# Performance work log

Measured on AMD Instinct MI355X. Metric: run time of the kernel, lower is better.

The kernel has to match this reference:

```python
import jax, jax.numpy as jnp
import numpy as np

B, D = 8192, 512
NB_CLASSES = 11318
N_EXP = 16
POS_THRESH = 0.25
TOP_K = int(round(B * POS_THRESH))  # plan==1: k = round(B * pos_thresh)


def make_bweights(n):
    # Deterministic init_bweights() from the torch module (17x17 for n=16).
    bw = np.zeros((n + 1, n + 1), dtype=np.float32)
    bw[:, 0] = -1.0 / n
    bw[0, 0] = 1.0
    for i in range(1, n + 1):
        for j in range(1, i):
            bw[i, j] = (-1.0 / n - bw[i] @ bw[j]) / bw[j, j]
        bw[i, i] = np.sqrt(1.0 - np.sum(bw[i, : i + 1] ** 2))
    bw[-1, -1] = 0.0
    return bw


def setup_inputs() -> dict:
    key = jax.random.key(0)
    k1, k2, k3, k4 = jax.random.split(key, 4)
    x_batch = jax.random.normal(k1, (B, D), jnp.float32)
    y_batch = jax.random.randint(k2, (B,), 0, NB_CLASSES)
    # kaiming_normal_ mode='fan_out' on a [nb_classes, sz_embed] tensor: std=sqrt(2/nb_classes)
    proxies = jax.random.normal(k3, (NB_CLASSES, D), jnp.float32) * np.float32(np.sqrt(2.0 / NB_CLASSES))
    rand_units = jax.random.normal(k4, (TOP_K, N_EXP, D), jnp.float32)
    rand_units = rand_units / jnp.linalg.norm(rand_units, axis=-1, keepdims=True)  # gen_unit()
    bweights = jnp.asarray(make_bweights(N_EXP))
    return {"x_batch": x_batch, "y_batch": y_batch, "proxies": proxies,
            "bweights": bweights, "rand_units": rand_units}


def _l2norm(x):
    # torch l2_norm: x / sqrt(sum(x^2, dim=1) + 1e-12)
    return x / jnp.sqrt(jnp.sum(x * x, axis=1, keepdims=True) + 1e-12)


def _expand_one(z, w_c, rands, bweights):
    # one2many_expansion for a single sample. z, w_c: [D]; rands: [N_EXP, D]
    M = jnp.dot(z, w_c) * w_c                 # projection onto class proxy
    r1 = z - M
    r1n = jnp.linalg.norm(r1)
    u1 = r1 / r1n
    # Build orthonormal basis v: [D, N_EXP+2]; columns 0,1 are w_c, u1,
    # columns 2.. via Gram-Schmidt on pre-drawn random unit vectors.
    v = jnp.zeros((D, N_EXP + 2), z.dtype).at[:, 0].set(w_c).at[:, 1].set(u1)
    for i in range(2, N_EXP + 2):  # fixed, small unrolled loop (16 steps)
        r = rands[i - 2]
        nb = r - v[:, :i] @ (v[:, :i].T @ r)  # == sum_j (r.b_j) b_j projection removal
        v = v.at[:, i].set(nb / jnp.linalg.norm(nb))
    # torch: v = v.clone().detach(); v[:,1] = u_1  (only u1 carries gradient)
    v = jax.lax.stop_gradient(v).at[:, 1].set(u1)
    u_rows = bweights @ v[:, 1:].T            # [N_EXP+1, D]
    z_exp = M[None, :] + u_rows * r1n         # [N_EXP+1, D]
    return z_exp[1:]                          # last N_EXP rows


def reference(x_batch, y_batch, proxies, bweights, rand_units):
    X = _l2norm(x_batch)                                  # keep_grad=True
    P = jax.lax.stop_gradient(_l2norm(proxies))           # .clone().detach()
    w = P[y_batch]                                        # [B, D] class proxies
    scores = jnp.sum(X * w, axis=1)                       # z @ P[lb]
    _, top_idx = jax.lax.top_k(scores, TOP_K)
    sel = jnp.sort(top_idx)  # torch loop appends expansions in ascending sample index order
    z_exp = jax.vmap(_expand_one, in_axes=(0, 0, 0, None))(X[sel], w[sel], rand_units, bweights)  # [TOP_K, N_EXP, D]
    lb_exp = jnp.repeat(y_batch[sel], N_EXP)
    aug_x = jnp.concatenate([x_batch, z_exp.reshape(-1, D)], axis=0)
    aug_t = jnp.concatenate([y_batch, lb_exp], axis=0)
    is_expan = jnp.zeros((B,), bool).at[sel].set(True)
    return aug_x, aug_t, is_expan
```

## Files before the change

### kernel.cpp

```cpp
#include <hip/hip_runtime.h>
#include <math.h>

#define BB     8192
#define DD     512
#define NEXP   16
#define TOPK   2048
#define AUGX_ROWS (BB + TOPK * NEXP)
#define AUGT_OFF  ((size_t)AUGX_ROWS * DD)
#define ISEXP_OFF (AUGT_OFF + AUGX_ROWS)

#define JCHUNK 256
#define COPY_BLOCKS 1024
#define BMP 520

typedef __attribute__((ext_vector_type(8)))  short bf16x8;
typedef __attribute__((ext_vector_type(16))) float f32x16;

__device__ inline ushort f2bf(float f) {
    uint u = __builtin_bit_cast(uint, f);
    return (ushort)((u + 0x7FFFu + ((u >> 16) & 1u)) >> 16);
}
__device__ inline float bf2f(ushort b) {
    uint u = ((uint)b) << 16;
    return __builtin_bit_cast(float, u);
}

__global__ __launch_bounds__(64) void score_kernel(
    const float* __restrict__ x, const int* __restrict__ y,
    const float* __restrict__ prox, double* __restrict__ scores)
{
    int i = blockIdx.x;
    int lane = threadIdx.x;
    const float* xr = x + (size_t)i * DD;
    const float* pr = prox + (size_t)y[i] * DD;
    double sx = 0.0, sp = 0.0, dp = 0.0;
    #pragma unroll
    for (int e = 0; e < DD; e += 64) {
        float xv = xr[e + lane];
        float pv = pr[e + lane];
        sx += (double)xv * (double)xv;
        sp += (double)pv * (double)pv;
        dp += (double)xv * (double)pv;
    }
    #pragma unroll
    for (int off = 32; off > 0; off >>= 1) {
        sx += __shfl_down(sx, off);
        sp += __shfl_down(sp, off);
        dp += __shfl_down(dp, off);
    }
    if (lane == 0) {
        scores[i] = dp / (sqrt(sx + 1e-12) * sqrt(sp + 1e-12));
    }
}

__global__ __launch_bounds__(256) void rank_kernel(
    const double* __restrict__ scores, int* __restrict__ ranks)
{
    __shared__ double ch[JCHUNK];
    int i = blockIdx.x * 256 + threadIdx.x;
    int jbase = blockIdx.y * JCHUNK;
    double si = scores[i];
    if (threadIdx.x < JCHUNK) ch[threadIdx.x] = scores[jbase + threadIdx.x];
    __syncthreads();
    int rank = 0;
    #pragma unroll 8
    for (int j = 0; j < JCHUNK; ++j) {
        double sj = ch[j];
        int jj = jbase + j;
        rank += (sj > si || (sj == si && jj < i)) ? 1 : 0;
    }
    atomicAdd(&ranks[i], rank);
}

__global__ __launch_bounds__(256) void compact_kernel(
    const int* __restrict__ ranks, int* __restrict__ sel, float* __restrict__ out)
{
    __shared__ int wsum[4];
    int t = threadIdx.x;
    int base = t * 32;
    int fl[32];
    int cnt = 0;
    for (int k = 0; k < 32; ++k) {
        fl[k] = (ranks[base + k] < TOPK) ? 1 : 0;
        cnt += fl[k];
    }
    int lane = t & 63, wave = t >> 6;
    int inc = cnt;
    #pragma unroll
    for (int off = 1; off < 64; off <<= 1) {
        int n = __shfl_up(inc, off);
        if (lane >= off) inc += n;
    }
    if (lane == 63) wsum[wave] = inc;
    __syncthreads();
    int wbase = 0;
    for (int w = 0; w < wave; ++w) wbase += wsum[w];
    int pos = wbase + inc - cnt;
    for (int k = 0; k < 32; ++k) {
        int i = base + k;
        out[ISEXP_OFF + i] = fl[k] ? 1.0f : 0.0f;
        if (fl[k]) sel[pos++] = i;
    }
}

__device__ inline void block_sum3(float& a, float& b, float& c, float* red, int t)
{
    #pragma unroll
    for (int off = 32; off > 0; off >>= 1) {
        a += __shfl_down(a, off);
        b += __shfl_down(b, off);
        c += __shfl_down(c, off);
    }
    __syncthreads();
    if ((t & 63) == 0) { int w = t >> 6; red[w] = a; red[4 + w] = b; red[8 + w] = c; }
    __syncthreads();
    a = red[0] + red[1] + red[2] + red[3];
    b = red[4] + red[5] + red[6] + red[7];
    c = red[8] + red[9] + red[10] + red[11];
}

__global__ __launch_bounds__(256, 6) void expand_kernel(
    const float* __restrict__ x, const int* __restrict__ y,
    const float* __restrict__ prox, const float* __restrict__ bwg,
    const float* __restrict__ rands, const int* __restrict__ sel,
    float* __restrict__ out)
{
    const int t = threadIdx.x;

    if (blockIdx.x >= TOPK) {
        int tid = (blockIdx.x - TOPK) * 256 + t;
        const float4* src = (const float4*)x;
        float4* dst = (float4*)out;
        const int nvec = BB * DD / 4;
        for (int idx = tid; idx < nvec; idx += COPY_BLOCKS * 256) dst[idx] = src[idx];
        for (int i = tid; i < BB; i += COPY_BLOCKS * 256) out[AUGT_OFF + i] = (float)y[i];
        return;
    }

    __shared__ ushort Bm[18][BMP];
    __shared__ float Gp[4][18][19];
    __shared__ float Ls[18][19];
    __shared__ float Cs[16][18];
    __shared__ float invd[18];
    __shared__ float red[12];

    const int j = blockIdx.x;
    const int wave = t >> 6, lane = t & 63;
    const int s = sel[j];
    const int cls = y[s];

    {
        const float* rbase = rands + (size_t)j * NEXP * DD;
        #pragma unroll
        for (int i = 0; i < 8; ++i) {
            int row = 2 * i + (t >> 7);
            int col = (t & 127) * 4;
            float4 vv = *(const float4*)(rbase + (size_t)row * DD + col);
            ushort4 bv = { f2bf(vv.x), f2bf(vv.y), f2bf(vv.z), f2bf(vv.w) };
            *(ushort4*)&Bm[2 + row][col] = bv;
        }
    }

    float2 xv = ((const float2*)(x + (size_t)s * DD))[t];
    float2 pv = ((const float2*)(prox + (size_t)cls * DD))[t];

    float sx  = xv.x * xv.x + xv.y * xv.y;
    float sp  = pv.x * pv.x + pv.y * pv.y;
    float dxp = xv.x * pv.x + xv.y * pv.y;
    block_sum3(sx, sp, dxp, red, t);

    float xn = sqrtf(sx + 1e-12f), pn = sqrtf(sp + 1e-12f);
    float2 z  = { xv.x / xn, xv.y / xn };
    float2 w  = { pv.x / pn, pv.y / pn };
    float zw  = dxp / (xn * pn);
    float2 M  = { zw * w.x, zw * w.y };
    float2 r1 = { z.x - M.x, z.y - M.y };
    float r1sq = fmaxf(1.0f - zw * zw, 1e-12f);
    float r1n = sqrtf(r1sq);
    float inv1 = 1.0f / r1n;
    float2 u1 = { r1.x * inv1, r1.y * inv1 };

    { ushort2 wb = { f2bf(w.x),  f2bf(w.y)  }; *(ushort2*)&Bm[0][2 * t] = wb; }
    { ushort2 ub = { f2bf(u1.x), f2bf(u1.y) }; *(ushort2*)&Bm[1][2 * t] = ub; }

    if (t < NEXP) out[AUGT_OFF + BB + (size_t)j * NEXP + t] = (float)cls;
    __syncthreads();

    {
        int row = lane & 31; if (row > 17) row = 17;
        int koff = (lane >> 5) * 8;
        const int kw = wave * 128;
        f32x16 acc = {0,0,0,0,0,0,0,0,0,0,0,0,0,0,0,0};
        #pragma unroll
        for (int stp = 0; stp < 8; ++stp) {
            bf16x8 av = *(const bf16x8*)&Bm[row][kw + stp * 16 + koff];
            acc = __builtin_amdgcn_mfma_f32_32x32x16_bf16(av, av, acc, 0, 0, 0);
        }
        int col = lane & 31;
        if (col < 18) {
            #pragma unroll
            for (int rg = 0; rg < 16; ++rg) {
                int rr = (rg & 3) + 8 * (rg >> 2) + 4 * (lane >> 5);
                if (rr < 18) Gp[wave][rr][col] = acc[rg];
            }
        }
    }
    __syncthreads();

    if (wave == 0) {
        const int jl = (lane < 18) ? lane : 17;
        float Greg[18];
        #pragma unroll
        for (int c = 0; c < 18; ++c)
            Greg[c] = (Gp[0][jl][c] + Gp[1][jl][c])
                    + (Gp[2][jl][c] + Gp[3][jl][c]);

        float Lrow[18], idr[18];
        #pragma unroll
        for (int col = 0; col < 18; ++col) {
            float pivot = __shfl(Greg[col], col);
            float rsq = rsqrtf(pivot);
            idr[col] = rsq;
            float lv = (jl >= col) ? Greg[col] * rsq : 0.0f;
            Lrow[col] = lv;
            #pragma unroll
            for (int c = col + 1; c < 18; ++c) {
                float lc = __shfl(lv, c);
                Greg[c] -= lv * lc;
            }
        }
        #pragma unroll
        for (int c = 0; c < 18; ++c) Ls[jl][c] = Lrow[c];
        if (lane < 18) invd[lane] = idr[lane];

        if (lane < 16) {
            float b[18];
            b[0] = 0.0f;
            #pragma unroll
            for (int m = 1; m < 18; ++m) b[m] = bwg[17 + lane * 17 + (m - 1)];
            #pragma unroll
            for (int k = 17; k >= 0; --k) {
                float xk = b[k] * idr[k];
                Cs[lane][k] = xk;
                #pragma unroll
                for (int m = 0; m < k; ++m)
                    b[m] -= Ls[k][m] * xk;
            }
        }
    }
    __syncthreads();

    float* orow = out + ((size_t)BB + (size_t)j * NEXP) * DD;
    #pragma unroll
    for (int half = 0; half < 2; ++half) {
        float acc0[8], acc1[8];
        #pragma unroll
        for (int r = 0; r < 8; ++r) { acc0[r] = 0.0f; acc1[r] = 0.0f; }
        #pragma unroll
        for (int jj = 0; jj < 18; ++jj) {
            float bx = bf2f(Bm[jj][2 * t]);
            float by = bf2f(Bm[jj][2 * t + 1]);
            #pragma unroll
            for (int r = 0; r < 8; ++r) {
                float cc = Cs[half * 8 + r][jj];
                acc0[r] += cc * bx;
                acc1[r] += cc * by;
            }
        }
        #pragma unroll
        for (int r = 0; r < 8; ++r) {
            float2 ov = { M.x + r1n * acc0[r], M.y + r1n * acc1[r] };
            ((float2*)(orow + (size_t)(half * 8 + r) * DD))[t] = ov;
        }
    }
}

extern "C" void kernel_launch(void* const* d_in, const int* in_sizes, int n_in,
                              void* d_out, int out_size, void* d_ws, size_t ws_size,
                              hipStream_t stream)
{
    const float* x     = (const float*)d_in[0];
    const int*   y     = (const int*)d_in[1];
    const float* prox  = (const float*)d_in[2];
    const float* bw    = (const float*)d_in[3];
    const float* rands = (const float*)d_in[4];
    float* out = (float*)d_out;

    char* wsb = (char*)d_ws;
    double* scores = (double*)wsb;
    int* ranks = (int*)(wsb + 65536);
    int* sel   = (int*)(wsb + 65536 + 32768);

    hipMemsetAsync(ranks, 0, BB * sizeof(int), stream);

    score_kernel<<<BB, 64, 0, stream>>>(x, y, prox, scores);
    dim3 rgrid(BB / 256, BB / JCHUNK);
    rank_kernel<<<rgrid, 256, 0, stream>>>(scores, ranks);
    compact_kernel<<<1, 256, 0, stream>>>(ranks, sel, out);
    expand_kernel<<<TOPK + COPY_BLOCKS, 256, 0, stream>>>(x, y, prox, bw, rands, sel, out);
}
```

Baseline: 71.97 us.

## Precompute per-sample norms in score kernel and split copy into separate kernel

```diff
diff --git a/kernel.cpp b/kernel.cpp
--- a/kernel.cpp
+++ b/kernel.cpp
@@ -10,7 +10,6 @@
 #define ISEXP_OFF (AUGT_OFF + AUGX_ROWS)
 
 #define JCHUNK 256
-#define COPY_BLOCKS 1024
 #define BMP 520
 
 typedef __attribute__((ext_vector_type(8)))  short bf16x8;
@@ -27,7 +26,8 @@
 
 __global__ __launch_bounds__(64) void score_kernel(
     const float* __restrict__ x, const int* __restrict__ y,
-    const float* __restrict__ prox, double* __restrict__ scores)
+    const float* __restrict__ prox, double* __restrict__ scores,
+    float4* __restrict__ hdr)
 {
     int i = blockIdx.x;
     int lane = threadIdx.x;
@@ -49,7 +49,13 @@
         dp += __shfl_down(dp, off);
     }
     if (lane == 0) {
-        scores[i] = dp / (sqrt(sx + 1e-12) * sqrt(sp + 1e-12));
+        double xn = sqrt(sx + 1e-12), pn = sqrt(sp + 1e-12);
+        double zw = dp / (xn * pn);
+        scores[i] = zw;
+        double r1sq = 1.0 - zw * zw;
+        if (r1sq < 1e-12) r1sq = 1e-12;
+        float4 h = { (float)xn, (float)pn, (float)zw, (float)sqrt(r1sq) };
+        hdr[i] = h;
     }
 }
 
@@ -103,47 +109,31 @@
     }
 }
 
-__device__ inline void block_sum3(float& a, float& b, float& c, float* red, int t)
-{
-    #pragma unroll
-    for (int off = 32; off > 0; off >>= 1) {
-        a += __shfl_down(a, off);
-        b += __shfl_down(b, off);
-        c += __shfl_down(c, off);
-    }
-    __syncthreads();
-    if ((t & 63) == 0) { int w = t >> 6; red[w] = a; red[4 + w] = b; red[8 + w] = c; }
-    __syncthreads();
-    a = red[0] + red[1] + red[2] + red[3];
-    b = red[4] + red[5] + red[6] + red[7];
-    c = red[8] + red[9] + red[10] + red[11];
+__global__ __launch_bounds__(256) void copy_kernel(
+    const float* __restrict__ x, const int* __restrict__ y, float* __restrict__ out)
+{
+    int tid = blockIdx.x * 256 + threadIdx.x;
+    const float4* src = (const float4*)x;
+    float4* dst = (float4*)out;
+    const int nvec = BB * DD / 4;
+    for (int idx = tid; idx < nvec; idx += gridDim.x * 256) dst[idx] = src[idx];
+    for (int i = tid; i < BB; i += gridDim.x * 256) out[AUGT_OFF + i] = (float)y[i];
 }
 
 __global__ __launch_bounds__(256, 6) void expand_kernel(
     const float* __restrict__ x, const int* __restrict__ y,
     const float* __restrict__ prox, const float* __restrict__ bwg,
     const float* __restrict__ rands, const int* __restrict__ sel,
-    float* __restrict__ out)
-{
+    const float4* __restrict__ hdr, float* __restrict__ out)
+{
+    __shared__ ushort Bm[18][BMP];
+    union SPool {
+        float Gp[4][18][19];
+        struct { float Ls[18][19]; float Cs[16][18]; } s;
+    };
+    __shared__ SPool pool;
+
     const int t = threadIdx.x;
-
-    if (blockIdx.x >= TOPK) {
-        int tid = (blockIdx.x - TOPK) * 256 + t;
-        const float4* src = (const float4*)x;
-        float4* dst = (float4*)out;
-        const int nvec = BB * DD / 4;
-        for (int idx = tid; idx < nvec; idx += COPY_BLOCKS * 256) dst[idx] = src[idx];
-        for (int i = tid; i < BB; i += COPY_BLOCKS * 256) out[AUGT_OFF + i] = (float)y[i];
-        return;
-    }
-
-    __shared__ ushort Bm[18][BMP];
-    __shared__ float Gp[4][18][19];
-    __shared__ float Ls[18][19];
-    __shared__ float Cs[16][18];
-    __shared__ float invd[18];
-    __shared__ float red[12];
-
     const int j = blockIdx.x;
     const int wave = t >> 6, lane = t & 63;
     const int s = sel[j];
@@ -161,24 +151,16 @@
         }
     }
 
+    float4 h = hdr[s];
+    const float zw = h.z, r1n = h.w;
+    const float ixn = 1.0f / h.x, ipn = 1.0f / h.y, ir1 = 1.0f / r1n;
+
     float2 xv = ((const float2*)(x + (size_t)s * DD))[t];
     float2 pv = ((const float2*)(prox + (size_t)cls * DD))[t];
-
-    float sx  = xv.x * xv.x + xv.y * xv.y;
-    float sp  = pv.x * pv.x + pv.y * pv.y;
-    float dxp = xv.x * pv.x + xv.y * pv.y;
-    block_sum3(sx, sp, dxp, red, t);
-
-    float xn = sqrtf(sx + 1e-12f), pn = sqrtf(sp + 1e-12f);
-    float2 z  = { xv.x / xn, xv.y / xn };
-    float2 w  = { pv.x / pn, pv.y / pn };
-    float zw  = dxp / (xn * pn);
+    float2 w  = { pv.x * ipn, pv.y * ipn };
+    float2 z  = { xv.x * ixn, xv.y * ixn };
     float2 M  = { zw * w.x, zw * w.y };
-    float2 r1 = { z.x - M.x, z.y - M.y };
-    float r1sq = fmaxf(1.0f - zw * zw, 1e-12f);
-    float r1n = sqrtf(r1sq);
-    float inv1 = 1.0f / r1n;
-    float2 u1 = { r1.x * inv1, r1.y * inv1 };
+    float2 u1 = { (z.x - M.x) * ir1, (z.y - M.y) * ir1 };
 
     { ushort2 wb = { f2bf(w.x),  f2bf(w.y)  }; *(ushort2*)&Bm[0][2 * t] = wb; }
     { ushort2 ub = { f2bf(u1.x), f2bf(u1.y) }; *(ushort2*)&Bm[1][2 * t] = ub; }
@@ -201,7 +183,7 @@
             #pragma unroll
             for (int rg = 0; rg < 16; ++rg) {
                 int rr = (rg & 3) + 8 * (rg >> 2) + 4 * (lane >> 5);
-                if (rr < 18) Gp[wave][rr][col] = acc[rg];
+                if (rr < 18) pool.Gp[wave][rr][col] = acc[rg];
             }
         }
     }
@@ -212,8 +194,8 @@
         float Greg[18];
         #pragma unroll
         for (int c = 0; c < 18; ++c)
-            Greg[c] = (Gp[0][jl][c] + Gp[1][jl][c])
-                    + (Gp[2][jl][c] + Gp[3][jl][c]);
+            Greg[c] = (pool.Gp[0][jl][c] + pool.Gp[1][jl][c])
+                    + (pool.Gp[2][jl][c] + pool.Gp[3][jl][c]);
 
         float Lrow[18], idr[18];
         #pragma unroll
@@ -230,8 +212,7 @@
             }
         }
         #pragma unroll
-        for (int c = 0; c < 18; ++c) Ls[jl][c] = Lrow[c];
-        if (lane < 18) invd[lane] = idr[lane];
+        for (int c = 0; c < 18; ++c) pool.s.Ls[jl][c] = Lrow[c];
 
         if (lane < 16) {
             float b[18];
@@ -241,10 +222,10 @@
             #pragma unroll
             for (int k = 17; k >= 0; --k) {
                 float xk = b[k] * idr[k];
-                Cs[lane][k] = xk;
+                pool.s.Cs[lane][k] = xk;
                 #pragma unroll
                 for (int m = 0; m < k; ++m)
-                    b[m] -= Ls[k][m] * xk;
+                    b[m] -= pool.s.Ls[k][m] * xk;
             }
         }
     }
@@ -262,7 +243,7 @@
             float by = bf2f(Bm[jj][2 * t + 1]);
             #pragma unroll
             for (int r = 0; r < 8; ++r) {
-                float cc = Cs[half * 8 + r][jj];
+                float cc = pool.s.Cs[half * 8 + r][jj];
                 acc0[r] += cc * bx;
                 acc1[r] += cc * by;
             }
@@ -290,12 +271,14 @@
     double* scores = (double*)wsb;
     int* ranks = (int*)(wsb + 65536);
     int* sel   = (int*)(wsb + 65536 + 32768);
+    float4* hdr = (float4*)(wsb + 114688);
 
     hipMemsetAsync(ranks, 0, BB * sizeof(int), stream);
 
-    score_kernel<<<BB, 64, 0, stream>>>(x, y, prox, scores);
+    score_kernel<<<BB, 64, 0, stream>>>(x, y, prox, scores, hdr);
     dim3 rgrid(BB / 256, BB / JCHUNK);
     rank_kernel<<<rgrid, 256, 0, stream>>>(scores, ranks);
     compact_kernel<<<1, 256, 0, stream>>>(ranks, sel, out);
-    expand_kernel<<<TOPK + COPY_BLOCKS, 256, 0, stream>>>(x, y, prox, bw, rands, sel, out);
-}
+    copy_kernel<<<512, 256, 0, stream>>>(x, y, out);
+    expand_kernel<<<TOPK, 256, 0, stream>>>(x, y, prox, bw, rands, sel, hdr, out);
+}
```

Measured after the change: 76.86 us. +6.8%, slower.
